# Kernel optimization log

Hardware: AMD Instinct MI355X
Metric: run time of the kernel (lower is better)

Reference implementation:

```python
import jax, jax.numpy as jnp
import numpy as np

T, B, D, H = 1024, 32, 256, 256


def _gru_scan(gi, whh, bhh, h0, reverse):
    # gi: (T, B, 3H) precomputed input projections; torch GRUCell gate order r,z,n
    def step(h, gi_t):
        gh = h @ whh.T + bhh
        ir, iz, inn = jnp.split(gi_t, 3, axis=-1)
        hr, hz, hn = jnp.split(gh, 3, axis=-1)
        r = jax.nn.sigmoid(ir + hr)
        z = jax.nn.sigmoid(iz + hz)
        n = jnp.tanh(inn + r * hn)
        h_new = (1.0 - z) * n + z * h
        return h_new, h_new
    _, ys = jax.lax.scan(step, h0, gi, reverse=reverse)
    return ys  # (T, B, H)


def _roll_seq(seq, shifts):
    # per-example roll along the time axis; seq: (T, B, *), shifts: (B,)
    return jax.vmap(lambda s, k: jnp.roll(s, k, axis=0), in_axes=(1, 0), out_axes=1)(seq, shifts)


def _layer(x, lengths, wih_f, whh_f, bih_f, bhh_f, wih_b, whh_b, bih_b, bhh_b):
    Tt, Bb = x.shape[0], x.shape[1]
    h0 = jnp.zeros((Bb, whh_f.shape[-1]), x.dtype)
    batch_ix = jnp.arange(Bb)
    # forward direction: scan over padded input (padding steps run too, as in torch code)
    gi_f = jnp.einsum('tbd,gd->tbg', x, wih_f) + bih_f
    ys_f = _gru_scan(gi_f, whh_f, bhh_f, h0, reverse=False)
    hn_f = ys_f[lengths - 1, batch_ix]  # state at last valid step
    # backward direction: align_sequence(shift_right=True) moves valid data to the end,
    # then a reversed scan; output is rolled back (shift left) afterwards.
    x_sh = _roll_seq(x, Tt - lengths)
    gi_b = jnp.einsum('tbd,gd->tbg', x_sh, wih_b) + bih_b
    ys_b = _gru_scan(gi_b, whh_b, bhh_b, h0, reverse=True)
    hn_b = ys_b[Tt - lengths, batch_ix]  # state after processing `length` reversed steps
    ys_b = _roll_seq(ys_b, -(Tt - lengths))
    # interleave dirs like torch.stack(dim=2).view(T, B, -1) -> concat [fwd, bwd]
    out = jnp.concatenate([ys_f[:, :, None, :], ys_b[:, :, None, :]], axis=2).reshape(Tt, Bb, -1)
    return out, hn_f, hn_b


def setup_inputs() -> dict:
    key = jax.random.key(0)
    ks = jax.random.split(key, 20)
    scale = 1.0 / np.sqrt(H)
    u = lambda k, shape: jax.random.uniform(k, shape, jnp.float32, -scale, scale)
    inp = {'x': jax.random.normal(ks[0], (T, B, D), jnp.float32)}
    i = 1
    for layer, in_dim in [('l0', D), ('l1', 2 * H)]:
        for d in ('f', 'b'):
            inp[f'w_ih_{layer}{d}'] = u(ks[i], (3 * H, in_dim)); i += 1
            inp[f'w_hh_{layer}{d}'] = u(ks[i], (3 * H, H)); i += 1
            inp[f'b_ih_{layer}{d}'] = u(ks[i], (3 * H,)); i += 1
            inp[f'b_hh_{layer}{d}'] = u(ks[i], (3 * H,)); i += 1
    lengths = jax.random.randint(ks[17], (B,), T // 2, T + 1)
    lengths = jnp.sort(lengths)[::-1].at[0].set(T).astype(jnp.int32)  # descending, max == T
    inp['lengths'] = lengths
    return inp


def reference(x,
              w_ih_l0f, w_hh_l0f, b_ih_l0f, b_hh_l0f,
              w_ih_l0b, w_hh_l0b, b_ih_l0b, b_hh_l0b,
              w_ih_l1f, w_hh_l1f, b_ih_l1f, b_hh_l1f,
              w_ih_l1b, w_hh_l1b, b_ih_l1b, b_hh_l1b,
              lengths):
    out0, h0f, h0b = _layer(x, lengths,
                            w_ih_l0f, w_hh_l0f, b_ih_l0f, b_hh_l0f,
                            w_ih_l0b, w_hh_l0b, b_ih_l0b, b_hh_l0b)
    # no inter-layer dropout (eval / dropout=0); layer output fed unmasked, as in torch code
    out1, h1f, h1b = _layer(out0, lengths,
                            w_ih_l1f, w_hh_l1f, b_ih_l1f, b_hh_l1f,
                            w_ih_l1b, w_hh_l1b, b_ih_l1b, b_hh_l1b)
    last_hidden = jnp.stack([h0f, h0b, h1f, h1b], axis=0)  # (L*2, B, H)
    indicator = (jnp.arange(out1.shape[0])[:, None] < lengths[None, :])[..., None]
    output = out1 * indicator.astype(out1.dtype)
    return output, last_hidden
```

## Files before the change

kernel.cpp:

```cpp
#include <hip/hip_runtime.h>
#include <hip/hip_bf16.h>
#include <hip/hip_fp16.h>

#define T_ 1024
#define B_ 32
#define H_ 256
#define G3 768

typedef _Float16 half2_t __attribute__((ext_vector_type(2)));

__device__ __forceinline__ float sigmoidf_(float x) { return 1.f / (1.f + __expf(-x)); }
__device__ __forceinline__ float tanhf_(float x) {
    float e = __expf(2.f * x);
    return (e - 1.f) / (e + 1.f);
}

__device__ __forceinline__ void sync_lds() {
    asm volatile("s_waitcnt lgkmcnt(0)" ::: "memory");
    asm volatile("s_barrier" ::: "memory");
}

__device__ __forceinline__ float fdot2_(unsigned int w, unsigned int h, float acc) {
#if __has_builtin(__builtin_amdgcn_fdot2)
    return __builtin_amdgcn_fdot2(__builtin_bit_cast(half2_t, w),
                                  __builtin_bit_cast(half2_t, h), acc, false);
#else
    half2_t a = __builtin_bit_cast(half2_t, w);
    half2_t b = __builtin_bit_cast(half2_t, h);
    return acc + (float)a[0] * (float)b[0] + (float)a[1] * (float)b[1];
#endif
}

__device__ __forceinline__ unsigned int pack_f16rn(float x, float y) {
    unsigned short ux = __half_as_ushort(__float2half_rn(x));
    unsigned short uy = __half_as_ushort(__float2half_rn(y));
    return (unsigned int)ux | ((unsigned int)uy << 16);
}

template <typename CT>
__global__ __launch_bounds__(256) void gemm_bias_nt(
    const float* __restrict__ A, const float* __restrict__ W,
    const float* __restrict__ bias, CT* __restrict__ C,
    int M, int N, int K)
{
    __shared__ float As[16][68];
    __shared__ float Ws[16][68];
    const int tid = threadIdx.x;
    const int bm = blockIdx.y * 64;
    const int bn = blockIdx.x * 64;
    const int lr = tid & 63;
    const int lc = tid >> 6;
    const int tx = tid & 15;
    const int ty = tid >> 4;

    const float* Ap = A + (size_t)(bm + lr) * K + lc * 4;
    const float* Wp = W + (size_t)(bn + lr) * K + lc * 4;

    float acc[4][4];
#pragma unroll
    for (int i = 0; i < 4; ++i)
#pragma unroll
        for (int j = 0; j < 4; ++j) acc[i][j] = 0.f;

    for (int k0 = 0; k0 < K; k0 += 16) {
        float4 av = *(const float4*)(Ap + k0);
        float4 wv = *(const float4*)(Wp + k0);
        __syncthreads();
        As[lc * 4 + 0][lr] = av.x; As[lc * 4 + 1][lr] = av.y;
        As[lc * 4 + 2][lr] = av.z; As[lc * 4 + 3][lr] = av.w;
        Ws[lc * 4 + 0][lr] = wv.x; Ws[lc * 4 + 1][lr] = wv.y;
        Ws[lc * 4 + 2][lr] = wv.z; Ws[lc * 4 + 3][lr] = wv.w;
        __syncthreads();
#pragma unroll
        for (int kk = 0; kk < 16; ++kk) {
            float4 a4 = *(const float4*)&As[kk][ty * 4];
            float4 w4 = *(const float4*)&Ws[kk][tx * 4];
            float am[4] = {a4.x, a4.y, a4.z, a4.w};
            float wn[4] = {w4.x, w4.y, w4.z, w4.w};
#pragma unroll
            for (int i = 0; i < 4; ++i)
#pragma unroll
                for (int j = 0; j < 4; ++j) acc[i][j] += am[i] * wn[j];
        }
    }

#pragma unroll
    for (int i = 0; i < 4; ++i) {
        size_t cbase = (size_t)(bm + ty * 4 + i) * N + bn + tx * 4;
#pragma unroll
        for (int j = 0; j < 4; ++j) {
            float v = acc[i][j] + bias[bn + tx * 4 + j];
            C[cbase + j] = (CT)v;
        }
    }
}

template <typename PT>
__global__ __launch_bounds__(512, 2) void gru_scan_reg(
    const PT* __restrict__ Pf, const PT* __restrict__ Pb,
    const float* __restrict__ Wf, const float* __restrict__ Wb,
    const float* __restrict__ bhf, const float* __restrict__ bhb,
    const int* __restrict__ lengths,
    float* __restrict__ out,
    float* __restrict__ hn,
    int do_mask)
{
    const int b = blockIdx.x >> 1;
    const int dir = blockIdx.x & 1;
    const PT* P = dir ? Pb : Pf;
    const float* W = dir ? Wb : Wf;
    const float* bh = dir ? bhb : bhf;
    const int len = lengths[b];

    __shared__ unsigned short h16s[H_];
    __shared__ float part[3][H_];

    const int tid = threadIdx.x;
    const int j = tid & 255;
    const int kh = tid >> 8;

    unsigned int wr[64], wz[64], wn[64];
    {
        const float4* r0 = (const float4*)(W + (size_t)j * H_ + kh * 128);
        const float4* r1 = (const float4*)(W + (size_t)(j + 256) * H_ + kh * 128);
        const float4* r2 = (const float4*)(W + (size_t)(j + 512) * H_ + kh * 128);
#pragma unroll
        for (int q = 0; q < 32; ++q) {
            float4 a = r0[q]; wr[2 * q] = pack_f16rn(a.x, a.y); wr[2 * q + 1] = pack_f16rn(a.z, a.w);
            float4 c = r1[q]; wz[2 * q] = pack_f16rn(c.x, c.y); wz[2 * q + 1] = pack_f16rn(c.z, c.w);
            float4 d = r2[q]; wn[2 * q] = pack_f16rn(d.x, d.y); wn[2 * q + 1] = pack_f16rn(d.z, d.w);
            __builtin_amdgcn_sched_barrier(0);
        }
    }

    float bh0 = 0.f, bh1 = 0.f, bh2 = 0.f;
    if (tid < H_) { bh0 = bh[j]; bh1 = bh[j + 256]; bh2 = bh[j + 512]; }

    float hreg = 0.f;
    if (tid < H_) h16s[tid] = 0;

    float* outp = out + (size_t)b * 512 + dir * 256;
    float* hnp = hn + (size_t)dir * (B_ * H_) + (size_t)b * H_;

    int crow = dir ? ((len - 1) & (T_ - 1)) : 0;
    int prow = dir ? ((len - 2) & (T_ - 1)) : 1;
    const int rstep = dir ? -1 : 1;
    const PT* Pbase = P + (size_t)b * G3 + j;

    float cir = 0.f, ciz = 0.f, cin = 0.f;
    if (tid < H_) {
        const PT* pp = Pbase + (size_t)crow * (B_ * G3);
        cir = (float)pp[0]; ciz = (float)pp[256]; cin = (float)pp[512];
    }
    sync_lds();

#pragma unroll 1
    for (int s = 0; s < T_; ++s) {
        float nir = 0.f, niz = 0.f, nin = 0.f;
        if (s + 1 < T_ && tid < H_) {
            const PT* pp = Pbase + (size_t)prow * (B_ * G3);
            nir = (float)pp[0]; niz = (float)pp[256]; nin = (float)pp[512];
        }

        float ar0 = 0.f, ar1 = 0.f, az0 = 0.f, az1 = 0.f, an0 = 0.f, an1 = 0.f;
        const uint4* hv = ((const uint4*)h16s) + kh * 16;
#pragma unroll
        for (int m = 0; m < 8; ++m) {
            uint4 ua = hv[2 * m];
            uint4 ub = hv[2 * m + 1];
            ar0 = fdot2_(wr[8 * m + 0], ua.x, ar0);
            az0 = fdot2_(wz[8 * m + 0], ua.x, az0);
            an0 = fdot2_(wn[8 * m + 0], ua.x, an0);
            ar1 = fdot2_(wr[8 * m + 1], ua.y, ar1);
            az1 = fdot2_(wz[8 * m + 1], ua.y, az1);
            an1 = fdot2_(wn[8 * m + 1], ua.y, an1);
            ar0 = fdot2_(wr[8 * m + 2], ua.z, ar0);
            az0 = fdot2_(wz[8 * m + 2], ua.z, az0);
            an0 = fdot2_(wn[8 * m + 2], ua.z, an0);
            ar1 = fdot2_(wr[8 * m + 3], ua.w, ar1);
            az1 = fdot2_(wz[8 * m + 3], ua.w, az1);
            an1 = fdot2_(wn[8 * m + 3], ua.w, an1);
            ar0 = fdot2_(wr[8 * m + 4], ub.x, ar0);
            az0 = fdot2_(wz[8 * m + 4], ub.x, az0);
            an0 = fdot2_(wn[8 * m + 4], ub.x, an0);
            ar1 = fdot2_(wr[8 * m + 5], ub.y, ar1);
            az1 = fdot2_(wz[8 * m + 5], ub.y, az1);
            an1 = fdot2_(wn[8 * m + 5], ub.y, an1);
            ar0 = fdot2_(wr[8 * m + 6], ub.z, ar0);
            az0 = fdot2_(wz[8 * m + 6], ub.z, az0);
            an0 = fdot2_(wn[8 * m + 6], ub.z, an0);
            ar1 = fdot2_(wr[8 * m + 7], ub.w, ar1);
            az1 = fdot2_(wz[8 * m + 7], ub.w, az1);
            an1 = fdot2_(wn[8 * m + 7], ub.w, an1);
            if (m & 1) __builtin_amdgcn_sched_barrier(0);
        }
        const float ar = ar0 + ar1;
        const float az = az0 + az1;
        const float an = an0 + an1;
        if (kh) {
            part[0][j] = ar;
            part[1][j] = az;
            part[2][j] = an;
        }
        sync_lds();

        if (tid < H_) {
            float gr = ar + part[0][j] + bh0;
            float gz = az + part[1][j] + bh1;
            float gn = an + part[2][j] + bh2;
            float r = sigmoidf_(cir + gr);
            float z = sigmoidf_(ciz + gz);
            float nn = tanhf_(cin + r * gn);
            float hnew = (1.f - z) * nn + z * hreg;
            hreg = hnew;
            h16s[j] = __half_as_ushort(__float2half_rn(hnew));
            float ov = (do_mask && crow >= len) ? 0.f : hnew;
            outp[(size_t)crow * (B_ * 512) + j] = ov;
            if (s == len - 1) hnp[j] = hnew;
        }
        sync_lds();

        cir = nir; ciz = niz; cin = nin;
        crow = (crow + rstep) & (T_ - 1);
        prow = (prow + rstep) & (T_ - 1);
    }
}

extern "C" void kernel_launch(void* const* d_in, const int* in_sizes, int n_in,
                              void* d_out, int out_size, void* d_ws, size_t ws_size,
                              hipStream_t stream)
{
    const float* x        = (const float*)d_in[0];
    const float* w_ih_l0f = (const float*)d_in[1];
    const float* w_hh_l0f = (const float*)d_in[2];
    const float* b_ih_l0f = (const float*)d_in[3];
    const float* b_hh_l0f = (const float*)d_in[4];
    const float* w_ih_l0b = (const float*)d_in[5];
    const float* w_hh_l0b = (const float*)d_in[6];
    const float* b_ih_l0b = (const float*)d_in[7];
    const float* b_hh_l0b = (const float*)d_in[8];
    const float* w_ih_l1f = (const float*)d_in[9];
    const float* w_hh_l1f = (const float*)d_in[10];
    const float* b_ih_l1f = (const float*)d_in[11];
    const float* b_hh_l1f = (const float*)d_in[12];
    const float* w_ih_l1b = (const float*)d_in[13];
    const float* w_hh_l1b = (const float*)d_in[14];
    const float* b_ih_l1b = (const float*)d_in[15];
    const float* b_hh_l1b = (const float*)d_in[16];
    const int*   lengths  = (const int*)d_in[17];

    float* out = (float*)d_out;
    const size_t OUT_OFF = (size_t)T_ * B_ * 512;
    float* hn0 = out + OUT_OFF;
    float* hn1 = hn0 + 2 * B_ * H_;

    const size_t PE = (size_t)T_ * B_ * G3;
    const int M = T_ * B_;
    dim3 gg(G3 / 64, M / 64);

    if (ws_size >= 2 * PE * sizeof(float)) {
        float* P0 = (float*)d_ws;
        float* P1 = P0 + PE;
        gemm_bias_nt<float><<<gg, 256, 0, stream>>>(x, w_ih_l0f, b_ih_l0f, P0, M, G3, 256);
        gemm_bias_nt<float><<<gg, 256, 0, stream>>>(x, w_ih_l0b, b_ih_l0b, P1, M, G3, 256);
        gru_scan_reg<float><<<64, 512, 0, stream>>>(P0, P1, w_hh_l0f, w_hh_l0b,
                                                    b_hh_l0f, b_hh_l0b, lengths, out, hn0, 0);
        gemm_bias_nt<float><<<gg, 256, 0, stream>>>(out, w_ih_l1f, b_ih_l1f, P0, M, G3, 512);
        gemm_bias_nt<float><<<gg, 256, 0, stream>>>(out, w_ih_l1b, b_ih_l1b, P1, M, G3, 512);
        gru_scan_reg<float><<<64, 512, 0, stream>>>(P0, P1, w_hh_l1f, w_hh_l1b,
                                                    b_hh_l1f, b_hh_l1b, lengths, out, hn1, 1);
    } else if (ws_size >= 2 * PE * sizeof(__hip_bfloat16)) {
        __hip_bfloat16* P0 = (__hip_bfloat16*)d_ws;
        __hip_bfloat16* P1 = P0 + PE;
        gemm_bias_nt<__hip_bfloat16><<<gg, 256, 0, stream>>>(x, w_ih_l0f, b_ih_l0f, P0, M, G3, 256);
        gemm_bias_nt<__hip_bfloat16><<<gg, 256, 0, stream>>>(x, w_ih_l0b, b_ih_l0b, P1, M, G3, 256);
        gru_scan_reg<__hip_bfloat16><<<64, 512, 0, stream>>>(P0, P1, w_hh_l0f, w_hh_l0b,
                                                             b_hh_l0f, b_hh_l0b, lengths, out, hn0, 0);
        gemm_bias_nt<__hip_bfloat16><<<gg, 256, 0, stream>>>(out, w_ih_l1f, b_ih_l1f, P0, M, G3, 512);
        gemm_bias_nt<__hip_bfloat16><<<gg, 256, 0, stream>>>(out, w_ih_l1b, b_ih_l1b, P1, M, G3, 512);
        gru_scan_reg<__hip_bfloat16><<<64, 512, 0, stream>>>(P0, P1, w_hh_l1f, w_hh_l1b,
                                                             b_hh_l1f, b_hh_l1b, lengths, out, hn1, 1);
    }
}
```

Baseline: 3.596 ms.

## Reduce GRU gate partial sums via wave shuffle and double-buffer hidden state

Remaps threads so the two K-halves of each hidden unit sit in lanes 32 apart of the same wave. The split-K partial sums are then combined with a cross-lane shuffle instead of an LDS exchange. The hidden-state buffer is double-buffered so one barrier per timestep can replace two. Every lane now loads the input projections and computes the gate nonlinearities redundantly, and only the lower half-wave writes results.

Result: slower. 3.676 ms (+2.2%).

```diff
diff --git a/kernel.cpp b/kernel.cpp
--- a/kernel.cpp
+++ b/kernel.cpp
@@ -96,7 +96,7 @@
 }
 
 template <typename PT>
-__global__ __launch_bounds__(512, 2) void gru_scan_reg(
+__global__ __launch_bounds__(512, 2) void gru_scan_shfl(
     const PT* __restrict__ Pf, const PT* __restrict__ Pb,
     const float* __restrict__ Wf, const float* __restrict__ Wb,
     const float* __restrict__ bhf, const float* __restrict__ bhb,
@@ -112,12 +112,13 @@
     const float* bh = dir ? bhb : bhf;
     const int len = lengths[b];
 
-    __shared__ unsigned short h16s[H_];
-    __shared__ float part[3][H_];
+    __shared__ __align__(16) unsigned short h16[2][H_];
 
     const int tid = threadIdx.x;
-    const int j = tid & 255;
-    const int kh = tid >> 8;
+    const int lane = tid & 63;
+    const int wave = tid >> 6;
+    const int j = wave * 32 + (lane & 31);
+    const int kh = lane >> 5;
 
     unsigned int wr[64], wz[64], wn[64];
     {
@@ -133,11 +134,12 @@
         }
     }
 
-    float bh0 = 0.f, bh1 = 0.f, bh2 = 0.f;
-    if (tid < H_) { bh0 = bh[j]; bh1 = bh[j + 256]; bh2 = bh[j + 512]; }
+    const float bh0 = bh[j];
+    const float bh1 = bh[j + 256];
+    const float bh2 = bh[j + 512];
 
     float hreg = 0.f;
-    if (tid < H_) h16s[tid] = 0;
+    if (tid < H_) h16[0][tid] = 0;
 
     float* outp = out + (size_t)b * 512 + dir * 256;
     float* hnp = hn + (size_t)dir * (B_ * H_) + (size_t)b * H_;
@@ -147,8 +149,8 @@
     const int rstep = dir ? -1 : 1;
     const PT* Pbase = P + (size_t)b * G3 + j;
 
-    float cir = 0.f, ciz = 0.f, cin = 0.f;
-    if (tid < H_) {
+    float cir, ciz, cin;
+    {
         const PT* pp = Pbase + (size_t)crow * (B_ * G3);
         cir = (float)pp[0]; ciz = (float)pp[256]; cin = (float)pp[512];
     }
@@ -157,13 +159,13 @@
 #pragma unroll 1
     for (int s = 0; s < T_; ++s) {
         float nir = 0.f, niz = 0.f, nin = 0.f;
-        if (s + 1 < T_ && tid < H_) {
+        if (s + 1 < T_) {
             const PT* pp = Pbase + (size_t)prow * (B_ * G3);
             nir = (float)pp[0]; niz = (float)pp[256]; nin = (float)pp[512];
         }
 
         float ar0 = 0.f, ar1 = 0.f, az0 = 0.f, az1 = 0.f, an0 = 0.f, an1 = 0.f;
-        const uint4* hv = ((const uint4*)h16s) + kh * 16;
+        const uint4* hv = ((const uint4*)h16[s & 1]) + kh * 16;
 #pragma unroll
         for (int m = 0; m < 8; ++m) {
             uint4 ua = hv[2 * m];
@@ -194,26 +196,21 @@
             an1 = fdot2_(wn[8 * m + 7], ub.w, an1);
             if (m & 1) __builtin_amdgcn_sched_barrier(0);
         }
-        const float ar = ar0 + ar1;
-        const float az = az0 + az1;
-        const float an = an0 + an1;
-        if (kh) {
-            part[0][j] = ar;
-            part[1][j] = az;
-            part[2][j] = an;
-        }
-        sync_lds();
-
-        if (tid < H_) {
-            float gr = ar + part[0][j] + bh0;
-            float gz = az + part[1][j] + bh1;
-            float gn = an + part[2][j] + bh2;
-            float r = sigmoidf_(cir + gr);
-            float z = sigmoidf_(ciz + gz);
-            float nn = tanhf_(cin + r * gn);
-            float hnew = (1.f - z) * nn + z * hreg;
-            hreg = hnew;
-            h16s[j] = __half_as_ushort(__float2half_rn(hnew));
+        float ar = ar0 + ar1;
+        float az = az0 + az1;
+        float an = an0 + an1;
+        ar += __shfl_xor(ar, 32);
+        az += __shfl_xor(az, 32);
+        an += __shfl_xor(an, 32);
+
+        float r = sigmoidf_(cir + ar + bh0);
+        float z = sigmoidf_(ciz + az + bh1);
+        float nn = tanhf_(cin + r * (an + bh2));
+        float hnew = (1.f - z) * nn + z * hreg;
+        hreg = hnew;
+
+        if (lane < 32) {
+            h16[(s & 1) ^ 1][j] = __half_as_ushort(__float2half_rn(hnew));
             float ov = (do_mask && crow >= len) ? 0.f : hnew;
             outp[(size_t)crow * (B_ * 512) + j] = ov;
             if (s == len - 1) hnp[j] = hnew;
@@ -263,22 +260,22 @@
         float* P1 = P0 + PE;
         gemm_bias_nt<float><<<gg, 256, 0, stream>>>(x, w_ih_l0f, b_ih_l0f, P0, M, G3, 256);
         gemm_bias_nt<float><<<gg, 256, 0, stream>>>(x, w_ih_l0b, b_ih_l0b, P1, M, G3, 256);
-        gru_scan_reg<float><<<64, 512, 0, stream>>>(P0, P1, w_hh_l0f, w_hh_l0b,
-                                                    b_hh_l0f, b_hh_l0b, lengths, out, hn0, 0);
+        gru_scan_shfl<float><<<64, 512, 0, stream>>>(P0, P1, w_hh_l0f, w_hh_l0b,
+                                                     b_hh_l0f, b_hh_l0b, lengths, out, hn0, 0);
         gemm_bias_nt<float><<<gg, 256, 0, stream>>>(out, w_ih_l1f, b_ih_l1f, P0, M, G3, 512);
         gemm_bias_nt<float><<<gg, 256, 0, stream>>>(out, w_ih_l1b, b_ih_l1b, P1, M, G3, 512);
-        gru_scan_reg<float><<<64, 512, 0, stream>>>(P0, P1, w_hh_l1f, w_hh_l1b,
-                                                    b_hh_l1f, b_hh_l1b, lengths, out, hn1, 1);
+        gru_scan_shfl<float><<<64, 512, 0, stream>>>(P0, P1, w_hh_l1f, w_hh_l1b,
+                                                     b_hh_l1f, b_hh_l1b, lengths, out, hn1, 1);
     } else if (ws_size >= 2 * PE * sizeof(__hip_bfloat16)) {
         __hip_bfloat16* P0 = (__hip_bfloat16*)d_ws;
         __hip_bfloat16* P1 = P0 + PE;
         gemm_bias_nt<__hip_bfloat16><<<gg, 256, 0, stream>>>(x, w_ih_l0f, b_ih_l0f, P0, M, G3, 256);
         gemm_bias_nt<__hip_bfloat16><<<gg, 256, 0, stream>>>(x, w_ih_l0b, b_ih_l0b, P1, M, G3, 256);
-        gru_scan_reg<__hip_bfloat16><<<64, 512, 0, stream>>>(P0, P1, w_hh_l0f, w_hh_l0b,
-                                                             b_hh_l0f, b_hh_l0b, lengths, out, hn0, 0);
+        gru_scan_shfl<__hip_bfloat16><<<64, 512, 0, stream>>>(P0, P1, w_hh_l0f, w_hh_l0b,
+                                                              b_hh_l0f, b_hh_l0b, lengths, out, hn0, 0);
         gemm_bias_nt<__hip_bfloat16><<<gg, 256, 0, stream>>>(out, w_ih_l1f, b_ih_l1f, P0, M, G3, 512);
         gemm_bias_nt<__hip_bfloat16><<<gg, 256, 0, stream>>>(out, w_ih_l1b, b_ih_l1b, P1, M, G3, 512);
-        gru_scan_reg<__hip_bfloat16><<<64, 512, 0, stream>>>(P0, P1, w_hh_l1f, w_hh_l1b,
-                                                             b_hh_l1f, b_hh_l1b, lengths, out, hn1, 1);
-    }
-}
+        gru_scan_shfl<__hip_bfloat16><<<64, 512, 0, stream>>>(P0, P1, w_hh_l1f, w_hh_l1b,
+                                                              b_hh_l1f, b_hh_l1b, lengths, out, hn1, 1);
+    }
+}
```
